# Optimization experiments

Hardware: AMD Instinct MI355X
Metric: run time of the kernel (lower is better)

The kernel has to match this reference:

```python
import jax, jax.numpy as jnp
import numpy as np

N, N_Z, N_C = 8192, 256, 128
DT = 0.1   # module-level dt in the original repo (RLS_prob * dt used as a probability)
TAU = 1.0  # self.tau


def setup_inputs() -> dict:
    key = jax.random.key(0)
    ks = jax.random.split(key, 12)
    g, p, w_tilde, b_tilde = 1.5, 0.1, 1.0, 0.2
    # recurrent weights: N(0, g/sqrt(p*N)) * Bernoulli(p) sparsity mask
    W_rr = jax.random.normal(ks[0], (N, N), jnp.float32) * (g / np.sqrt(p * N))
    W_rr = W_rr * (jax.random.uniform(ks[1], (N, N)) < p).astype(jnp.float32)
    W_zr = jax.random.uniform(ks[2], (N, N_Z), jnp.float32, -w_tilde, w_tilde)
    W_cr = jax.random.uniform(ks[3], (N, N_C), jnp.float32, -w_tilde, w_tilde)
    W_epsr = jax.random.uniform(ks[4], (N, N_Z), jnp.float32, -w_tilde, w_tilde)
    # readouts are zero-initialized in the original; use small random values so the
    # step (and its gradients) are non-trivial, as they would be mid-training
    W_rz = 0.01 * jax.random.normal(ks[5], (N_Z, N), jnp.float32)
    W_rc = 0.01 * jax.random.normal(ks[6], (N_C, N), jnp.float32)
    b = jax.random.uniform(ks[7], (N,), jnp.float32, -b_tilde, b_tilde)
    x = jax.random.normal(ks[8], (N,), jnp.float32)
    eps = jax.random.normal(ks[9], (N_Z,), jnp.float32)
    c = jax.random.normal(ks[10], (N_C,), jnp.float32)
    z_tilde = jax.random.normal(ks[11], (N_Z,), jnp.float32)
    return {"x": x, "eps": eps, "c": c, "z_tilde": z_tilde,
            "W_rr": W_rr, "W_zr": W_zr, "W_cr": W_cr, "W_epsr": W_epsr,
            "W_rz": W_rz, "W_rc": W_rc, "b": b}


def reference(x, eps, c, z_tilde, W_rr, W_zr, W_cr, W_epsr, W_rz, W_rc, b):
    # current firing rate and readout (r = tanh(x+b), z = r_z(r) hold after every step)
    r = jnp.tanh(x + b)
    z = W_rz @ r
    # Euler step: x += dt*(-x + W_rr r + W_epsr eps + W_zr z + W_cr c)/tau
    dx = -x + W_rr @ r + W_epsr @ eps + W_zr @ z + W_cr @ c
    x_new = x + DT * dx / TAU
    r_new = jnp.tanh(x_new + b)
    z_new = W_rz @ r_new
    c_new = W_rc @ r_new
    eps_new = z_new - z_tilde
    # concat of [x_new (N), r_new (N), z_new (N_z), c_new (N_c), eps_new (N_z)]
    return jnp.concatenate([x_new, r_new, z_new, c_new, eps_new])
```

## Files before the change

### kernel.cpp

```cpp
#include <hip/hip_runtime.h>
#include <math.h>

#define N   8192
#define NZ  256
#define NC  128
#define DT  0.1f

typedef float fx4 __attribute__((ext_vector_type(4)));

__device__ __forceinline__ float wave_reduce(float v) {
    #pragma unroll
    for (int off = 32; off > 0; off >>= 1)
        v += __shfl_down(v, off, 64);
    return v;
}

__device__ __forceinline__ float dot4v(fx4 a, fx4 b) {
    return a.x * b.x + a.y * b.y + a.z * b.z + a.w * b.w;
}

__device__ __forceinline__ fx4 ntload4(const float* p) {
    return __builtin_nontemporal_load((const fx4*)p);
}
__device__ __forceinline__ fx4 ld4(const float* p) {
    return *(const fx4*)p;
}

__global__ __launch_bounds__(256) void k1_r(const float* __restrict__ x,
                                            const float* __restrict__ b,
                                            float* __restrict__ r) {
    int i = blockIdx.x * blockDim.x + threadIdx.x;
    fx4 xv = ld4(x + 4 * i), bv = ld4(b + 4 * i), rv;
    rv.x = tanhf(xv.x + bv.x);
    rv.y = tanhf(xv.y + bv.y);
    rv.z = tanhf(xv.z + bv.z);
    rv.w = tanhf(xv.w + bv.w);
    *(fx4*)(r + 4 * i) = rv;
}

__device__ __forceinline__ float block_row_dot(const float* __restrict__ row,
                                               const float* __restrict__ v) {
    int t = threadIdx.x;
    float acc = 0.f;
    #pragma unroll
    for (int j = 0; j < (N / 4) / 256; ++j) {
        int idx = 4 * (t + j * 256);
        acc += dot4v(ntload4(row + idx), ld4(v + idx));
    }
    acc = wave_reduce(acc);
    __shared__ float part[4];
    int wave = t >> 6, lane = t & 63;
    if (lane == 0) part[wave] = acc;
    __syncthreads();
    return part[0] + part[1] + part[2] + part[3];
}

__global__ __launch_bounds__(256) void k2_z(const float* __restrict__ Wrz,
                                            const float* __restrict__ r,
                                            float* __restrict__ z) {
    int row = blockIdx.x;
    float d = block_row_dot(Wrz + (size_t)row * N, r);
    if (threadIdx.x == 0) z[row] = d;
}

__global__ __launch_bounds__(256) void k3_main(const float* __restrict__ Wrr,
                                               const float* __restrict__ Wepsr,
                                               const float* __restrict__ Wzr,
                                               const float* __restrict__ Wcr,
                                               const float* __restrict__ r,
                                               const float* __restrict__ eps,
                                               const float* __restrict__ z,
                                               const float* __restrict__ c,
                                               const float* __restrict__ x,
                                               const float* __restrict__ b,
                                               float* __restrict__ out) {
    int row  = (blockIdx.x * blockDim.x + threadIdx.x) >> 6;
    int lane = threadIdx.x & 63;
    if (row >= N) return;

    const float* wr = Wrr + (size_t)row * N;
    float acc = 0.f;
    #pragma unroll 16
    for (int k = 0; k < (N / 4) / 64; ++k) {
        int idx = 4 * (lane + k * 64);
        acc += dot4v(ntload4(wr + idx), ld4(r + idx));
    }
    {
        acc += dot4v(ntload4(Wepsr + (size_t)row * NZ + 4 * lane),
                     ld4(eps + 4 * lane));
    }
    {
        acc += dot4v(ntload4(Wzr + (size_t)row * NZ + 4 * lane),
                     ld4(z + 4 * lane));
    }
    if (lane < NC / 4) {
        acc += dot4v(ntload4(Wcr + (size_t)row * NC + 4 * lane),
                     ld4(c + 4 * lane));
    }
    acc = wave_reduce(acc);
    if (lane == 0) {
        float xi = x[row];
        float dx = acc - xi;
        float xn = xi + DT * dx;
        float rn = tanhf(xn + b[row]);
        out[row]     = xn;
        out[N + row] = rn;
    }
}

__global__ __launch_bounds__(256) void k4_heads(const float* __restrict__ Wrz,
                                                const float* __restrict__ Wrc,
                                                const float* __restrict__ rnew,
                                                const float* __restrict__ ztilde,
                                                float* __restrict__ out) {
    int row = blockIdx.x;
    const float* Wrow = (row < NZ) ? (Wrz + (size_t)row * N)
                                   : (Wrc + (size_t)(row - NZ) * N);
    float d = block_row_dot(Wrow, rnew);
    if (threadIdx.x == 0) {
        if (row < NZ) {
            out[2 * N + row]           = d;
            out[2 * N + NZ + NC + row] = d - ztilde[row];
        } else {
            out[2 * N + NZ + (row - NZ)] = d;
        }
    }
}

extern "C" void kernel_launch(void* const* d_in, const int* in_sizes, int n_in,
                              void* d_out, int out_size, void* d_ws, size_t ws_size,
                              hipStream_t stream) {
    const float* x      = (const float*)d_in[0];
    const float* eps    = (const float*)d_in[1];
    const float* c      = (const float*)d_in[2];
    const float* ztilde = (const float*)d_in[3];
    const float* Wrr    = (const float*)d_in[4];
    const float* Wzr    = (const float*)d_in[5];
    const float* Wcr    = (const float*)d_in[6];
    const float* Wepsr  = (const float*)d_in[7];
    const float* Wrz    = (const float*)d_in[8];
    const float* Wrc    = (const float*)d_in[9];
    const float* b      = (const float*)d_in[10];
    float* out = (float*)d_out;

    float* r = (float*)d_ws;
    float* z = r + N;

    k1_r<<<N / (256 * 4), 256, 0, stream>>>(x, b, r);
    k2_z<<<NZ, 256, 0, stream>>>(Wrz, r, z);
    k3_main<<<(N * 64) / 256, 256, 0, stream>>>(Wrr, Wepsr, Wzr, Wcr,
                                                r, eps, z, c, x, b, out);
    k4_heads<<<NZ + NC, 256, 0, stream>>>(Wrz, Wrc, out + N, ztilde, out);
}
```

Before: 378.0 us.

## Split recurrent matvec so W_rr work runs concurrently with z readout

```diff
diff --git a/kernel.cpp b/kernel.cpp
--- a/kernel.cpp
+++ b/kernel.cpp
@@ -26,9 +26,9 @@
     return *(const fx4*)p;
 }
 
-__global__ __launch_bounds__(256) void k1_r(const float* __restrict__ x,
-                                            const float* __restrict__ b,
-                                            float* __restrict__ r) {
+__global__ __launch_bounds__(64) void k1_r(const float* __restrict__ x,
+                                           const float* __restrict__ b,
+                                           float* __restrict__ r) {
     int i = blockIdx.x * blockDim.x + threadIdx.x;
     fx4 xv = ld4(x + 4 * i), bv = ld4(b + 4 * i), rv;
     rv.x = tanhf(xv.x + bv.x);
@@ -38,6 +38,71 @@
     *(fx4*)(r + 4 * i) = rv;
 }
 
+__global__ __launch_bounds__(256) void k3a(const float* __restrict__ Wrr,
+                                           const float* __restrict__ Wepsr,
+                                           const float* __restrict__ Wcr,
+                                           const float* __restrict__ Wrz,
+                                           const float* __restrict__ r,
+                                           const float* __restrict__ eps,
+                                           const float* __restrict__ c,
+                                           float* __restrict__ z,
+                                           float* __restrict__ accv) {
+    int wave = threadIdx.x >> 6, lane = threadIdx.x & 63;
+
+    if (blockIdx.x < NZ / 4) {
+        int row = blockIdx.x * 4 + wave;
+        const float* wr = Wrz + (size_t)row * N;
+        float acc = 0.f;
+        #pragma unroll 8
+        for (int k = 0; k < (N / 4) / 64; ++k) {
+            int idx = 4 * (lane + k * 64);
+            acc += dot4v(ld4(wr + idx), ld4(r + idx));
+        }
+        acc = wave_reduce(acc);
+        if (lane == 0) z[row] = acc;
+    } else {
+        int row = (blockIdx.x - NZ / 4) * 4 + wave;
+        const float* wr = Wrr + (size_t)row * N;
+        float acc = 0.f;
+        #pragma unroll 16
+        for (int k = 0; k < (N / 4) / 64; ++k) {
+            int idx = 4 * (lane + k * 64);
+            acc += dot4v(ntload4(wr + idx), ld4(r + idx));
+        }
+        {
+            acc += dot4v(ntload4(Wepsr + (size_t)row * NZ + 4 * lane),
+                         ld4(eps + 4 * lane));
+        }
+        if (lane < NC / 4) {
+            acc += dot4v(ntload4(Wcr + (size_t)row * NC + 4 * lane),
+                         ld4(c + 4 * lane));
+        }
+        acc = wave_reduce(acc);
+        if (lane == 0) accv[row] = acc;
+    }
+}
+
+__global__ __launch_bounds__(256) void k3b(const float* __restrict__ Wzr,
+                                           const float* __restrict__ z,
+                                           const float* __restrict__ accv,
+                                           const float* __restrict__ x,
+                                           const float* __restrict__ b,
+                                           float* __restrict__ out) {
+    int row  = (blockIdx.x * blockDim.x + threadIdx.x) >> 6;
+    int lane = threadIdx.x & 63;
+    float t = dot4v(ntload4(Wzr + (size_t)row * NZ + 4 * lane),
+                    ld4(z + 4 * lane));
+    t = wave_reduce(t);
+    if (lane == 0) {
+        float xi = x[row];
+        float dx = accv[row] + t - xi;
+        float xn = xi + DT * dx;
+        float rn = tanhf(xn + b[row]);
+        out[row]     = xn;
+        out[N + row] = rn;
+    }
+}
+
 __device__ __forceinline__ float block_row_dot(const float* __restrict__ row,
                                                const float* __restrict__ v) {
     int t = threadIdx.x;
@@ -45,7 +110,7 @@
     #pragma unroll
     for (int j = 0; j < (N / 4) / 256; ++j) {
         int idx = 4 * (t + j * 256);
-        acc += dot4v(ntload4(row + idx), ld4(v + idx));
+        acc += dot4v(ld4(row + idx), ld4(v + idx));
     }
     acc = wave_reduce(acc);
     __shared__ float part[4];
@@ -53,59 +118,6 @@
     if (lane == 0) part[wave] = acc;
     __syncthreads();
     return part[0] + part[1] + part[2] + part[3];
-}
-
-__global__ __launch_bounds__(256) void k2_z(const float* __restrict__ Wrz,
-                                            const float* __restrict__ r,
-                                            float* __restrict__ z) {
-    int row = blockIdx.x;
-    float d = block_row_dot(Wrz + (size_t)row * N, r);
-    if (threadIdx.x == 0) z[row] = d;
-}
-
-__global__ __launch_bounds__(256) void k3_main(const float* __restrict__ Wrr,
-                                               const float* __restrict__ Wepsr,
-                                               const float* __restrict__ Wzr,
-                                               const float* __restrict__ Wcr,
-                                               const float* __restrict__ r,
-                                               const float* __restrict__ eps,
-                                               const float* __restrict__ z,
-                                               const float* __restrict__ c,
-                                               const float* __restrict__ x,
-                                               const float* __restrict__ b,
-                                               float* __restrict__ out) {
-    int row  = (blockIdx.x * blockDim.x + threadIdx.x) >> 6;
-    int lane = threadIdx.x & 63;
-    if (row >= N) return;
-
-    const float* wr = Wrr + (size_t)row * N;
-    float acc = 0.f;
-    #pragma unroll 16
-    for (int k = 0; k < (N / 4) / 64; ++k) {
-        int idx = 4 * (lane + k * 64);
-        acc += dot4v(ntload4(wr + idx), ld4(r + idx));
-    }
-    {
-        acc += dot4v(ntload4(Wepsr + (size_t)row * NZ + 4 * lane),
-                     ld4(eps + 4 * lane));
-    }
-    {
-        acc += dot4v(ntload4(Wzr + (size_t)row * NZ + 4 * lane),
-                     ld4(z + 4 * lane));
-    }
-    if (lane < NC / 4) {
-        acc += dot4v(ntload4(Wcr + (size_t)row * NC + 4 * lane),
-                     ld4(c + 4 * lane));
-    }
-    acc = wave_reduce(acc);
-    if (lane == 0) {
-        float xi = x[row];
-        float dx = acc - xi;
-        float xn = xi + DT * dx;
-        float rn = tanhf(xn + b[row]);
-        out[row]     = xn;
-        out[N + row] = rn;
-    }
 }
 
 __global__ __launch_bounds__(256) void k4_heads(const float* __restrict__ Wrz,
@@ -143,12 +155,13 @@
     const float* b      = (const float*)d_in[10];
     float* out = (float*)d_out;
 
-    float* r = (float*)d_ws;
-    float* z = r + N;
+    float* r    = (float*)d_ws;
+    float* z    = r + N;
+    float* accv = z + NZ;
 
-    k1_r<<<N / (256 * 4), 256, 0, stream>>>(x, b, r);
-    k2_z<<<NZ, 256, 0, stream>>>(Wrz, r, z);
-    k3_main<<<(N * 64) / 256, 256, 0, stream>>>(Wrr, Wepsr, Wzr, Wcr,
-                                                r, eps, z, c, x, b, out);
+    k1_r<<<N / (64 * 4), 64, 0, stream>>>(x, b, r);
+    k3a<<<NZ / 4 + N / 4, 256, 0, stream>>>(Wrr, Wepsr, Wcr, Wrz,
+                                            r, eps, c, z, accv);
+    k3b<<<N / 4, 256, 0, stream>>>(Wzr, z, accv, x, b, out);
     k4_heads<<<NZ + NC, 256, 0, stream>>>(Wrz, Wrc, out + N, ztilde, out);
 }
```

New measurement: 379.2 us. No clear change (+0.3%).
